# Optimization experiments

Measured on AMD Instinct MI355X. Metric: run time of the kernel, lower is better.

## Reference

```python
import jax, jax.numpy as jnp
import numpy as np

B, T, U = 64, 800, 80          # batch, stroke timesteps, char sequence length
IN, H, V = 3, 400, 57          # input_dim, hidden_dim, onehot_dim (vocab)
K, G = 10, 20                  # n_window, n_gaussian
D1 = H + IN + V                # input dim of recurrent layers >= 1


def setup_inputs() -> dict:
    key = jax.random.key(0)
    ks = jax.random.split(key, 12)
    std = 0.075
    nrm = lambda k, shp: (std * jax.random.normal(k, shp)).astype(jnp.float32)
    char_ids = jax.random.randint(ks[1], (B, U), 0, V)
    return {
        "x_input": jax.random.normal(ks[0], (B, T, IN), jnp.float32),
        "onehot": jax.nn.one_hot(char_ids, V, dtype=jnp.float32),
        "h0": jnp.zeros((B, H), jnp.float32),
        "h1": jnp.zeros((B, H), jnp.float32),
        "h2": jnp.zeros((B, H), jnp.float32),
        # GRU layer 0 (input: strokes only)
        "W_ih0": nrm(ks[2], (3 * H, IN)), "W_hh0": nrm(ks[3], (3 * H, H)),
        "b_ih0": jnp.zeros((3 * H,), jnp.float32), "b_hh0": jnp.zeros((3 * H,), jnp.float32),
        # GRU layer 1 (shared by all layers >= 1, faithful to the torch code which
        # always calls self.rnn_layer1 in the loop)
        "W_ih1": nrm(ks[4], (3 * H, D1)), "W_hh1": nrm(ks[5], (3 * H, H)),
        "b_ih1": jnp.zeros((3 * H,), jnp.float32), "b_hh1": jnp.zeros((3 * H,), jnp.float32),
        # attention window linear: hidden -> 3*K (alpha, beta, kappa); bias ~ N(-4, 0.1)
        "W_win": nrm(ks[6], (3 * K, H)),
        "b_win": (-4.0 + 0.1 * jax.random.normal(ks[7], (3 * K,))).astype(jnp.float32),
        # MDN head: hidden -> 1 + 6*G
        "W_mdn": nrm(ks[8], (1 + 6 * G, H)),
        "b_mdn": jnp.zeros((1 + 6 * G,), jnp.float32),
    }


def gru(x, h0, W_ih, W_hh, b_ih, b_hh):
    """PyTorch-convention GRU. x: (B,T,D), h0: (B,H) -> (out (B,T,H), hT (B,H))."""
    xg = jnp.einsum('btd,gd->btg', x, W_ih) + b_ih  # (B,T,3H), precomputed input gates

    def step(h, xg_t):
        gh = h @ W_hh.T + b_hh
        xr, xz, xn = jnp.split(xg_t, 3, axis=-1)
        hr, hz, hn = jnp.split(gh, 3, axis=-1)
        r = jax.nn.sigmoid(xr + hr)
        z = jax.nn.sigmoid(xz + hz)
        n = jnp.tanh(xn + r * hn)
        h_new = (1.0 - z) * n + z * h
        return h_new, h_new

    hT, outs = jax.lax.scan(step, h0, jnp.swapaxes(xg, 0, 1))
    return jnp.swapaxes(outs, 0, 1), hT


def reference(x_input, onehot, h0, h1, h2,
              W_ih0, W_hh0, b_ih0, b_hh0,
              W_ih1, W_hh1, b_ih1, b_hh1,
              W_win, b_win, W_mdn, b_mdn):
    out0, _ = gru(x_input, h0, W_ih0, W_hh0, b_ih0, b_hh0)  # (B,T,H)

    # Graves attention window (training=True path: running_kappa = cumsum(kappa))
    abk = jnp.exp(out0 @ W_win.T + b_win)                    # (B,T,3K)
    alpha, beta, kappa = jnp.split(abk, 3, axis=-1)          # each (B,T,K)
    running_kappa = jnp.cumsum(kappa, axis=1)                # (B,T,K)
    u = jnp.arange(onehot.shape[1], dtype=x_input.dtype)     # (U,)
    diff = running_kappa[..., None] - u                      # (B,T,K,U)
    phi = jnp.sum(alpha[..., None] * jnp.exp(-beta[..., None] * diff * diff), axis=2)  # (B,T,U)
    window = jnp.einsum('btu,buv->btv', phi, onehot)         # (B,T,V)

    # layers >= 1 all use layer-1 weights (faithful to original torch code)
    out = jnp.concatenate([out0, window, x_input], axis=-1)
    out, _ = gru(out, h1, W_ih1, W_hh1, b_ih1, b_hh1)
    out = jnp.concatenate([out, window, x_input], axis=-1)
    out, _ = gru(out, h2, W_ih1, W_hh1, b_ih1, b_hh1)

    mdn = out.reshape(-1, H) @ W_mdn.T + b_mdn               # (B*T, 1+6G)
    pi_logit = mdn[:, 0 * G:1 * G]
    mu1 = mdn[:, 1 * G:2 * G]
    mu2 = mdn[:, 2 * G:3 * G]
    log_sigma1 = mdn[:, 3 * G:4 * G]
    log_sigma2 = mdn[:, 4 * G:5 * G]
    rho = jnp.tanh(mdn[:, 5 * G:6 * G])
    e_logit = mdn[:, 6 * G:]
    return jnp.concatenate([pi_logit, mu1, mu2, log_sigma1, log_sigma2, rho, e_logit], axis=-1)
```

## Files before the change

### kernel.cpp

```cpp
#include <hip/hip_runtime.h>
#include <math.h>

#define Bx 64
#define Tx 800
#define Ux 80
#define INx 3
#define Hx 400
#define Vx 57
#define Kx 10


typedef float v2f __attribute__((ext_vector_type(2)));
typedef float v4f __attribute__((ext_vector_type(4)));

__device__ __forceinline__ float sigf(float x) { return 1.f / (1.f + expf(-x)); }

__device__ __forceinline__ void pk_lo(v2f& acc, v2f w, v2f h) {
    asm("v_pk_fma_f32 %0, %1, %2, %0 op_sel:[0,0,0] op_sel_hi:[0,1,1]"
        : "+v"(acc) : "v"(w), "v"(h));
}
__device__ __forceinline__ void pk_hi(v2f& acc, v2f w, v2f h) {
    asm("v_pk_fma_f32 %0, %1, %2, %0 op_sel:[1,0,0] op_sel_hi:[1,1,1]"
        : "+v"(acc) : "v"(w), "v"(h));
}

__global__ void k_zero(int* __restrict__ cnt) {
    int i = blockIdx.x * blockDim.x + threadIdx.x;
    if (i < 3 * 16 * 32) cnt[i] = 0;
}

__global__ void k_transpose_x(const float* __restrict__ x, float* __restrict__ xT) {
    int idx = blockIdx.x * blockDim.x + threadIdx.x;
    if (idx >= Tx * INx * Bx) return;
    int b = idx & 63;
    int d = (idx >> 6) % INx;
    int t = idx / (64 * INx);
    xT[idx] = x[((size_t)b * Tx + t) * INx + d];
}

__global__ void k_transpose_oh(const float* __restrict__ oh, float* __restrict__ ohT) {
    int idx = blockIdx.x * blockDim.x + threadIdx.x;
    if (idx >= Ux * Vx * Bx) return;
    int b = idx & 63;
    int uv = idx >> 6;
    int v = uv % Vx;
    int u = uv / Vx;
    ohT[idx] = oh[((size_t)b * Ux + u) * Vx + v];
}

__global__ void k_packW(const float* __restrict__ Whh, const float* __restrict__ Wih,
                        float* __restrict__ Wp, int NP, int xcols) {
    int idx = blockIdx.x * blockDim.x + threadIdx.x;
    int total = 16 * 3 * NP * 400;
    if (idx >= total) return;
    int q = idx % 400;
    int m = (idx / 400) % (3 * NP);
    int us = idx / (400 * 3 * NP);
    int g = m / NP, p = m % NP;
    int s = q / 25, u = q % 25;
    int row = g * 400 + us * 25 + u;
    float v0, v1;
    if (p < 13) {
        int kl0 = 2 * p, kl1 = 2 * p + 1;
        v0 = (kl0 < 25) ? Whh[(size_t)row * 400 + s * 25 + kl0] : 0.f;
        v1 = (kl1 < 25) ? Whh[(size_t)row * 400 + s * 25 + kl1] : 0.f;
    } else {
        int jx0 = 2 * (p - 13), jx1 = jx0 + 1;
        int kx0 = s * 29 + jx0, kx1 = s * 29 + jx1;
        v0 = (jx0 < 29 && kx0 < xcols) ? Wih[(size_t)row * xcols + kx0] : 0.f;
        v1 = (jx1 < 29 && kx1 < xcols) ? Wih[(size_t)row * xcols + kx1] : 0.f;
    }
    Wp[(size_t)idx * 2]     = v0;
    Wp[(size_t)idx * 2 + 1] = v1;
}

template <int XP>
__global__ __launch_bounds__(448, 2) void k_rec(
    const float* __restrict__ Wp, const float* __restrict__ prev,
    const float* __restrict__ winb, const float* __restrict__ xT,
    const float* __restrict__ hinit, const float* __restrict__ Wih_small,
    const float* __restrict__ bih, const float* __restrict__ bhh,
    float* __restrict__ outL, int* __restrict__ cnt) {
    constexpr int NP = 13 + XP;
    constexpr int XW = (XP > 0) ? 466 : 4;
    __shared__ __align__(16) float xcat_h[404 * 4];
    __shared__ __align__(16) float xcat_x[2][XW * 4];
    __shared__ v2f red2[8 * 400];
    __shared__ float biasLDS[150];
    __shared__ float wih0LDS[225];

    const int tid = threadIdx.x;
    const int us = blockIdx.x >> 4;
    const int cg = blockIdx.x & 15;
    const int cb = cg * 4;
    const int U0 = us * 25;
    const int q = tid;
    const int s = q / 25;
    int* cnt_cg = cnt + cg * 32;

    v2f w[3 * NP];
    if (q < 400) {
        const v2f* Wp2 = (const v2f*)Wp;
        #pragma unroll
        for (int m = 0; m < 3 * NP; ++m)
            w[m] = Wp2[((size_t)(us * 3 * NP) + m) * 400 + q];
    } else {
        #pragma unroll
        for (int m = 0; m < 3 * NP; ++m) w[m] = (v2f){0.f, 0.f};
    }
    if (tid < 75)        biasLDS[tid] = bih[(tid / 25) * 400 + U0 + (tid % 25)];
    else if (tid < 150)  biasLDS[tid] = bhh[((tid - 75) / 25) * 400 + U0 + ((tid - 75) % 25)];
    if (XP == 0 && tid < 225) {
        int u = tid / 9, r9 = tid % 9, g = r9 / 3, d = r9 % 3;
        wih0LDS[tid] = Wih_small[(size_t)(g * 400 + U0 + u) * 3 + d];
    }
    for (int k = tid; k < 404; k += 448)
        *(v4f*)&xcat_h[k * 4] = (v4f){0.f, 0.f, 0.f, 0.f};
    for (int k = tid; k < 2 * XW; k += 448)
        *(v4f*)&xcat_x[0][k * 4] = (v4f){0.f, 0.f, 0.f, 0.f};
    __syncthreads();

    if (XP > 0) {
        for (int kx = tid; kx < 460; kx += 448) {
            v4f xv;
            if (kx < 400)      xv = *(const v4f*)(prev + (size_t)kx * 64 + cb);
            else if (kx < 457) xv = *(const v4f*)(winb + (size_t)(kx - 400) * 64 + cb);
            else               xv = *(const v4f*)(xT + (size_t)(kx - 457) * 64 + cb);
            *(v4f*)&xcat_x[0][kx * 4] = xv;
        }
    } else {
        if (tid < 3)
            *(v4f*)&xcat_x[0][tid * 4] = *(const v4f*)(xT + (size_t)tid * 64 + cb);
    }

    for (int t = 0; t < Tx; ++t) {
        const int pl = t & 1;
        if (tid < 400) {
            v4f hv;
            if (t == 0) {
                hv.x = hinit[(size_t)(cb + 0) * 400 + tid];
                hv.y = hinit[(size_t)(cb + 1) * 400 + tid];
                hv.z = hinit[(size_t)(cb + 2) * 400 + tid];
                hv.w = hinit[(size_t)(cb + 3) * 400 + tid];
            } else {
                float* hp0 = outL + (size_t)(t - 1) * 25600 + (size_t)tid * 64 + cb;
                hv.x = __hip_atomic_load(hp0 + 0, __ATOMIC_RELAXED, __HIP_MEMORY_SCOPE_AGENT);
                hv.y = __hip_atomic_load(hp0 + 1, __ATOMIC_RELAXED, __HIP_MEMORY_SCOPE_AGENT);
                hv.z = __hip_atomic_load(hp0 + 2, __ATOMIC_RELAXED, __HIP_MEMORY_SCOPE_AGENT);
                hv.w = __hip_atomic_load(hp0 + 3, __ATOMIC_RELAXED, __HIP_MEMORY_SCOPE_AGENT);
            }
            *(v4f*)&xcat_h[tid * 4] = hv;
        }
        __syncthreads();

        if (q < 400) {
            v2f aR0 = {0, 0}, aR1 = {0, 0}, aZ0 = {0, 0}, aZ1 = {0, 0};
            v2f aHN0 = {0, 0}, aHN1 = {0, 0}, aXN0 = {0, 0}, aXN1 = {0, 0};
            const float* hb = &xcat_h[s * 100];
            #pragma unroll
            for (int p = 0; p < 13; ++p) {
                v2f a01 = *(const v2f*)(hb + 8 * p);
                v2f a23 = *(const v2f*)(hb + 8 * p + 2);
                v2f b01 = *(const v2f*)(hb + 8 * p + 4);
                v2f b23 = *(const v2f*)(hb + 8 * p + 6);
                v2f wr = w[p], wz = w[NP + p], wn = w[2 * NP + p];
                pk_lo(aR0, wr, a01);  pk_lo(aR1, wr, a23);
                pk_hi(aR0, wr, b01);  pk_hi(aR1, wr, b23);
                pk_lo(aZ0, wz, a01);  pk_lo(aZ1, wz, a23);
                pk_hi(aZ0, wz, b01);  pk_hi(aZ1, wz, b23);
                pk_lo(aHN0, wn, a01); pk_lo(aHN1, wn, a23);
                pk_hi(aHN0, wn, b01); pk_hi(aHN1, wn, b23);
            }
            if (XP > 0) {
                const float* xb = &xcat_x[pl][s * 29 * 4];
                #pragma unroll
                for (int p = 0; p < XP; ++p) {
                    v2f a01 = *(const v2f*)(xb + 8 * p);
                    v2f a23 = *(const v2f*)(xb + 8 * p + 2);
                    v2f b01 = *(const v2f*)(xb + 8 * p + 4);
                    v2f b23 = *(const v2f*)(xb + 8 * p + 6);
                    v2f wr = w[13 + p], wz = w[NP + 13 + p], wn = w[2 * NP + 13 + p];
                    pk_lo(aR0, wr, a01);  pk_lo(aR1, wr, a23);
                    pk_hi(aR0, wr, b01);  pk_hi(aR1, wr, b23);
                    pk_lo(aZ0, wz, a01);  pk_lo(aZ1, wz, a23);
                    pk_hi(aZ0, wz, b01);  pk_hi(aZ1, wz, b23);
                    pk_lo(aXN0, wn, a01); pk_lo(aXN1, wn, a23);
                    pk_hi(aXN0, wn, b01); pk_hi(aXN1, wn, b23);
                }
            }
            red2[0 * 400 + q] = aR0;  red2[1 * 400 + q] = aR1;
            red2[2 * 400 + q] = aZ0;  red2[3 * 400 + q] = aZ1;
            red2[4 * 400 + q] = aHN0; red2[5 * 400 + q] = aHN1;
            red2[6 * 400 + q] = aXN0; red2[7 * 400 + q] = aXN1;
        }
        __syncthreads();

        if (tid < 100) {
            int u = tid >> 2, c = tid & 3;
            int half = c >> 1, e = c & 1;
            const float* redf = (const float*)red2;
            float R = 0, Z = 0, HN = 0, XN = 0;
            #pragma unroll 4
            for (int s2 = 0; s2 < 16; ++s2) {
                int idx = s2 * 25 + u;
                R  += redf[((0 + half) * 400 + idx) * 2 + e];
                Z  += redf[((2 + half) * 400 + idx) * 2 + e];
                HN += redf[((4 + half) * 400 + idx) * 2 + e];
                XN += redf[((6 + half) * 400 + idx) * 2 + e];
            }
            R += biasLDS[u] + biasLDS[75 + u];
            Z += biasLDS[25 + u] + biasLDS[100 + u];
            XN += biasLDS[50 + u];
            HN += biasLDS[125 + u];
            if (XP == 0) {
                #pragma unroll
                for (int d = 0; d < 3; ++d) {
                    float xv = xcat_x[pl][d * 4 + c];
                    R  += wih0LDS[u * 9 + 0 + d] * xv;
                    Z  += wih0LDS[u * 9 + 3 + d] * xv;
                    XN += wih0LDS[u * 9 + 6 + d] * xv;
                }
            }
            float r = sigf(R);
            float z = sigf(Z);
            float n = tanhf(XN + r * HN);
            float hp = xcat_h[(U0 + u) * 4 + c];
            float hnew = (1.f - z) * n + z * hp;
            __hip_atomic_store(outL + (size_t)t * 25600 + (size_t)(U0 + u) * 64 + cb + c,
                               hnew, __ATOMIC_RELAXED, __HIP_MEMORY_SCOPE_AGENT);
        }

        if (t + 1 < Tx) {
            const int p2 = (t + 1) & 1;
            if (XP > 0) {
                for (int kx = tid; kx < 460; kx += 448) {
                    v4f xv;
                    if (kx < 400)      xv = *(const v4f*)(prev + (size_t)(t + 1) * 25600 + kx * 64 + cb);
                    else if (kx < 457) xv = *(const v4f*)(winb + (size_t)(t + 1) * 3648 + (kx - 400) * 64 + cb);
                    else               xv = *(const v4f*)(xT + (size_t)(t + 1) * 192 + (kx - 457) * 64 + cb);
                    *(v4f*)&xcat_x[p2][kx * 4] = xv;
                }
            } else {
                if (tid < 3)
                    *(v4f*)&xcat_x[p2][tid * 4] = *(const v4f*)(xT + (size_t)(t + 1) * 192 + tid * 64 + cb);
            }
        }
        __syncthreads();

        if (tid == 0) {
            __hip_atomic_fetch_add(cnt_cg, 1, __ATOMIC_RELAXED, __HIP_MEMORY_SCOPE_AGENT);
            int target = 16 * (t + 1);
            while (__hip_atomic_load(cnt_cg, __ATOMIC_RELAXED, __HIP_MEMORY_SCOPE_AGENT) < target)
                __builtin_amdgcn_s_sleep(2);
        }
        __syncthreads();
    }
}

__global__ __launch_bounds__(256) void k_abk(const float* __restrict__ out0,
    const float* __restrict__ Wwin, const float* __restrict__ bwin,
    float* __restrict__ abk) {
    int t = blockIdx.x;
    int b = threadIdx.x & 63;
    int js = threadIdx.x >> 6;
    int j0 = js * 8;
    int nj = min(8, 30 - j0);
    float acc[8];
    for (int i = 0; i < nj; i++) acc[i] = bwin[j0 + i];
    const float* o = out0 + (size_t)t * 25600;
    for (int k = 0; k < Hx; k++) {
        float hv = o[k * 64 + b];
        for (int i = 0; i < nj; i++) acc[i] += Wwin[(j0 + i) * Hx + k] * hv;
    }
    for (int i = 0; i < nj; i++)
        abk[(size_t)t * 1920 + (j0 + i) * 64 + b] = expf(acc[i]);
}

__global__ void k_cumsum(float* __restrict__ abk) {
    int tid = blockIdx.x * blockDim.x + threadIdx.x;
    if (tid >= Kx * Bx) return;
    int b = tid & 63;
    int k = tid >> 6;
    float run = 0.f;
    size_t base = (size_t)(20 + k) * 64 + b;
    for (int t = 0; t < Tx; t++) {
        size_t i = (size_t)t * 1920 + base;
        run += abk[i];
        abk[i] = run;
    }
}

__global__ __launch_bounds__(256) void k_window(const float* __restrict__ abk,
    const float* __restrict__ ohT, float* __restrict__ win) {
    int t = blockIdx.x;
    int b = threadIdx.x & 63;
    int sub = threadIdx.x >> 6;
    __shared__ float phi[Ux][64];

    float al[Kx], be[Kx], kc[Kx];
    const float* ab = abk + (size_t)t * 1920;
    #pragma unroll
    for (int k = 0; k < Kx; k++) {
        al[k] = ab[k * 64 + b];
        be[k] = ab[(10 + k) * 64 + b];
        kc[k] = ab[(20 + k) * 64 + b];
    }
    for (int u = sub * 20; u < sub * 20 + 20; u++) {
        float ssum = 0.f;
        float uf = (float)u;
        #pragma unroll
        for (int k = 0; k < Kx; k++) {
            float d = kc[k] - uf;
            ssum += al[k] * __expf(-be[k] * d * d);
        }
        phi[u][b] = ssum;
    }
    __syncthreads();

    int v0 = sub * 15;
    int nv = min(15, Vx - v0);
    float acc[15];
    for (int i = 0; i < nv; i++) acc[i] = 0.f;
    for (int u = 0; u < Ux; u++) {
        float pv = phi[u][b];
        const float* oh = ohT + (size_t)(u * Vx) * 64;
        for (int i = 0; i < nv; i++) acc[i] += pv * oh[(v0 + i) * 64 + b];
    }
    for (int i = 0; i < nv; i++)
        win[(size_t)t * 3648 + (v0 + i) * 64 + b] = acc[i];
}

__global__ __launch_bounds__(256) void k_mdn(const float* __restrict__ out2,
    const float* __restrict__ Wm, const float* __restrict__ bm,
    float* __restrict__ out) {
    int t = blockIdx.x;
    int b = threadIdx.x & 63;
    int js = threadIdx.x >> 6;
    int j0 = js * 31;
    int nj = min(31, 121 - j0);
    float acc[31];
    for (int i = 0; i < nj; i++) acc[i] = bm[j0 + i];
    const float* o = out2 + (size_t)t * 25600;
    for (int k = 0; k < Hx; k += 4) {
        float i0 = o[k * 64 + b];
        float i1 = o[(k + 1) * 64 + b];
        float i2 = o[(k + 2) * 64 + b];
        float i3 = o[(k + 3) * 64 + b];
        for (int i = 0; i < nj; i++) {
            const float* wp = Wm + (size_t)(j0 + i) * Hx + k;
            float4 qv = *(const float4*)wp;
            acc[i] += qv.x * i0 + qv.y * i1 + qv.z * i2 + qv.w * i3;
        }
    }
    size_t rb = ((size_t)b * Tx + t) * 121;
    for (int i = 0; i < nj; i++) {
        int j = j0 + i;
        float v = acc[i];
        if (j >= 100 && j < 120) v = tanhf(v);
        out[rb + j] = v;
    }
}

extern "C" void kernel_launch(void* const* d_in, const int* in_sizes, int n_in,
                              void* d_out, int out_size, void* d_ws, size_t ws_size,
                              hipStream_t stream) {
    const float* x    = (const float*)d_in[0];
    const float* oneh = (const float*)d_in[1];
    const float* h0i  = (const float*)d_in[2];
    const float* h1i  = (const float*)d_in[3];
    const float* h2i  = (const float*)d_in[4];
    const float* Wih0 = (const float*)d_in[5];
    const float* Whh0 = (const float*)d_in[6];
    const float* bih0 = (const float*)d_in[7];
    const float* bhh0 = (const float*)d_in[8];
    const float* Wih1 = (const float*)d_in[9];
    const float* Whh1 = (const float*)d_in[10];
    const float* bih1 = (const float*)d_in[11];
    const float* bhh1 = (const float*)d_in[12];
    const float* Wwin = (const float*)d_in[13];
    const float* bwin = (const float*)d_in[14];
    const float* Wmdn = (const float*)d_in[15];
    const float* bmdn = (const float*)d_in[16];

    float* ws    = (float*)d_ws;
    float* out0  = ws;
    float* out12 = ws + 20480000;
    float* winb  = ws + 40960000;
    float* abk   = ws + 43878400;
    float* xT    = ws + 45414400;
    float* ohT   = ws + 45568000;
    float* Wp0   = ws + 45859840;
    float* Wp12  = ws + 46359040;
    int*   cnt   = (int*)(ws + 47434240);

    hipLaunchKernelGGL(k_zero, dim3(6), dim3(256), 0, stream, cnt);
    hipLaunchKernelGGL(k_transpose_x, dim3((Tx * INx * Bx + 255) / 256), dim3(256), 0, stream, x, xT);
    hipLaunchKernelGGL(k_transpose_oh, dim3((Ux * Vx * Bx + 255) / 256), dim3(256), 0, stream, oneh, ohT);
    hipLaunchKernelGGL(k_packW, dim3((16 * 3 * 13 * 400 + 255) / 256), dim3(256), 0, stream,
                       Whh0, Wih0, Wp0, 13, 3);
    hipLaunchKernelGGL(k_packW, dim3((16 * 3 * 28 * 400 + 255) / 256), dim3(256), 0, stream,
                       Whh1, Wih1, Wp12, 28, 460);

    hipLaunchKernelGGL((k_rec<0>), dim3(256), dim3(448), 0, stream,
                       Wp0, (const float*)nullptr, (const float*)nullptr, xT,
                       h0i, Wih0, bih0, bhh0, out0, cnt + 0 * 512);

    hipLaunchKernelGGL(k_abk, dim3(Tx), dim3(256), 0, stream, out0, Wwin, bwin, abk);
    hipLaunchKernelGGL(k_cumsum, dim3(10), dim3(64), 0, stream, abk);
    hipLaunchKernelGGL(k_window, dim3(Tx), dim3(256), 0, stream, abk, ohT, winb);

    hipLaunchKernelGGL((k_rec<15>), dim3(256), dim3(448), 0, stream,
                       Wp12, out0, winb, xT, h1i, (const float*)nullptr,
                       bih1, bhh1, out12, cnt + 1 * 512);
    hipLaunchKernelGGL((k_rec<15>), dim3(256), dim3(448), 0, stream,
                       Wp12, out12, winb, xT, h2i, (const float*)nullptr,
                       bih1, bhh1, out0, cnt + 2 * 512);

    hipLaunchKernelGGL(k_mdn, dim3(Tx), dim3(256), 0, stream, out0, Wmdn, bmdn, (float*)d_out);
}
```

Baseline: 14.58 ms.

## Replace counter barrier with per-wave flag polling in recurrent GRU kernel

Replaces the per-step atomic-add counter and tid0 spin plus two block barriers with per-wave flags. The two compute waves each store the step index once their h outputs drain, and every wave polls all 32 flags with a wave vote before loading h. The previous h for the gate update now comes from a double-buffered LDS copy, and h is loaded with a cache-bypassing dwordx4. The next-step x prefetch moves to the otherwise idle waves so it overlaps the gate math. Launch bounds drop to one block per CU. This removes two __syncthreads per step and a contended atomic, at the cost of more subtle memory-ordering correctness.

After: 16.38 ms. +12.3%, slower.

```diff
diff --git a/kernel.cpp b/kernel.cpp
--- a/kernel.cpp
+++ b/kernel.cpp
@@ -75,7 +75,7 @@
 }
 
 template <int XP>
-__global__ __launch_bounds__(448, 2) void k_rec(
+__global__ __launch_bounds__(448, 1) void k_rec(
     const float* __restrict__ Wp, const float* __restrict__ prev,
     const float* __restrict__ winb, const float* __restrict__ xT,
     const float* __restrict__ hinit, const float* __restrict__ Wih_small,
@@ -85,6 +85,7 @@
     constexpr int XW = (XP > 0) ? 466 : 4;
     __shared__ __align__(16) float xcat_h[404 * 4];
     __shared__ __align__(16) float xcat_x[2][XW * 4];
+    __shared__ __align__(16) float hprev[2][104 * 4];
     __shared__ v2f red2[8 * 400];
     __shared__ float biasLDS[150];
     __shared__ float wih0LDS[225];
@@ -118,7 +119,6 @@
         *(v4f*)&xcat_h[k * 4] = (v4f){0.f, 0.f, 0.f, 0.f};
     for (int k = tid; k < 2 * XW; k += 448)
         *(v4f*)&xcat_x[0][k * 4] = (v4f){0.f, 0.f, 0.f, 0.f};
-    __syncthreads();
 
     if (XP > 0) {
         for (int kx = tid; kx < 460; kx += 448) {
@@ -135,6 +135,14 @@
 
     for (int t = 0; t < Tx; ++t) {
         const int pl = t & 1;
+        if (t > 0) {
+            int* fp = cnt_cg + (tid & 31);
+            int fv = __hip_atomic_load(fp, __ATOMIC_RELAXED, __HIP_MEMORY_SCOPE_AGENT);
+            while (!__all(fv >= t)) {
+                __builtin_amdgcn_s_sleep(1);
+                fv = __hip_atomic_load(fp, __ATOMIC_RELAXED, __HIP_MEMORY_SCOPE_AGENT);
+            }
+        }
         if (tid < 400) {
             v4f hv;
             if (t == 0) {
@@ -143,13 +151,14 @@
                 hv.z = hinit[(size_t)(cb + 2) * 400 + tid];
                 hv.w = hinit[(size_t)(cb + 3) * 400 + tid];
             } else {
-                float* hp0 = outL + (size_t)(t - 1) * 25600 + (size_t)tid * 64 + cb;
-                hv.x = __hip_atomic_load(hp0 + 0, __ATOMIC_RELAXED, __HIP_MEMORY_SCOPE_AGENT);
-                hv.y = __hip_atomic_load(hp0 + 1, __ATOMIC_RELAXED, __HIP_MEMORY_SCOPE_AGENT);
-                hv.z = __hip_atomic_load(hp0 + 2, __ATOMIC_RELAXED, __HIP_MEMORY_SCOPE_AGENT);
-                hv.w = __hip_atomic_load(hp0 + 3, __ATOMIC_RELAXED, __HIP_MEMORY_SCOPE_AGENT);
+                const float* hp0 = outL + (size_t)(t - 1) * 25600 + (size_t)tid * 64 + cb;
+                asm volatile("global_load_dwordx4 %0, %1, off sc0 sc1"
+                             : "=v"(hv) : "v"(hp0) : "memory");
+                asm volatile("s_waitcnt vmcnt(0)" ::: "memory");
             }
             *(v4f*)&xcat_h[tid * 4] = hv;
+            int d = tid - U0;
+            if ((unsigned)d < 25u) *(v4f*)&hprev[t & 1][d * 4] = hv;
         }
         __syncthreads();
 
@@ -195,45 +204,49 @@
         }
         __syncthreads();
 
-        if (tid < 100) {
-            int u = tid >> 2, c = tid & 3;
-            int half = c >> 1, e = c & 1;
-            const float* redf = (const float*)red2;
-            float R = 0, Z = 0, HN = 0, XN = 0;
-            #pragma unroll 4
-            for (int s2 = 0; s2 < 16; ++s2) {
-                int idx = s2 * 25 + u;
-                R  += redf[((0 + half) * 400 + idx) * 2 + e];
-                Z  += redf[((2 + half) * 400 + idx) * 2 + e];
-                HN += redf[((4 + half) * 400 + idx) * 2 + e];
-                XN += redf[((6 + half) * 400 + idx) * 2 + e];
-            }
-            R += biasLDS[u] + biasLDS[75 + u];
-            Z += biasLDS[25 + u] + biasLDS[100 + u];
-            XN += biasLDS[50 + u];
-            HN += biasLDS[125 + u];
-            if (XP == 0) {
-                #pragma unroll
-                for (int d = 0; d < 3; ++d) {
-                    float xv = xcat_x[pl][d * 4 + c];
-                    R  += wih0LDS[u * 9 + 0 + d] * xv;
-                    Z  += wih0LDS[u * 9 + 3 + d] * xv;
-                    XN += wih0LDS[u * 9 + 6 + d] * xv;
+        if (tid < 128) {
+            if (tid < 100) {
+                int u = tid >> 2, c = tid & 3;
+                int half = c >> 1, e = c & 1;
+                const float* redf = (const float*)red2;
+                float R = 0, Z = 0, HN = 0, XN = 0;
+                #pragma unroll 4
+                for (int s2 = 0; s2 < 16; ++s2) {
+                    int idx = s2 * 25 + u;
+                    R  += redf[((0 + half) * 400 + idx) * 2 + e];
+                    Z  += redf[((2 + half) * 400 + idx) * 2 + e];
+                    HN += redf[((4 + half) * 400 + idx) * 2 + e];
+                    XN += redf[((6 + half) * 400 + idx) * 2 + e];
                 }
-            }
-            float r = sigf(R);
-            float z = sigf(Z);
-            float n = tanhf(XN + r * HN);
-            float hp = xcat_h[(U0 + u) * 4 + c];
-            float hnew = (1.f - z) * n + z * hp;
-            __hip_atomic_store(outL + (size_t)t * 25600 + (size_t)(U0 + u) * 64 + cb + c,
-                               hnew, __ATOMIC_RELAXED, __HIP_MEMORY_SCOPE_AGENT);
-        }
-
-        if (t + 1 < Tx) {
+                R += biasLDS[u] + biasLDS[75 + u];
+                Z += biasLDS[25 + u] + biasLDS[100 + u];
+                XN += biasLDS[50 + u];
+                HN += biasLDS[125 + u];
+                if (XP == 0) {
+                    #pragma unroll
+                    for (int d = 0; d < 3; ++d) {
+                        float xv = xcat_x[pl][d * 4 + c];
+                        R  += wih0LDS[u * 9 + 0 + d] * xv;
+                        Z  += wih0LDS[u * 9 + 3 + d] * xv;
+                        XN += wih0LDS[u * 9 + 6 + d] * xv;
+                    }
+                }
+                float r = sigf(R);
+                float z = sigf(Z);
+                float n = tanhf(XN + r * HN);
+                float hp = hprev[t & 1][u * 4 + c];
+                float hnew = (1.f - z) * n + z * hp;
+                __hip_atomic_store(outL + (size_t)t * 25600 + (size_t)(U0 + u) * 64 + cb + c,
+                                   hnew, __ATOMIC_RELAXED, __HIP_MEMORY_SCOPE_AGENT);
+            }
+            asm volatile("s_waitcnt vmcnt(0)" ::: "memory");
+            if ((tid & 63) == 0)
+                __hip_atomic_store(cnt_cg + us * 2 + (tid >> 6), t + 1,
+                                   __ATOMIC_RELAXED, __HIP_MEMORY_SCOPE_AGENT);
+        } else if (t + 1 < Tx) {
             const int p2 = (t + 1) & 1;
             if (XP > 0) {
-                for (int kx = tid; kx < 460; kx += 448) {
+                for (int kx = tid - 128; kx < 460; kx += 320) {
                     v4f xv;
                     if (kx < 400)      xv = *(const v4f*)(prev + (size_t)(t + 1) * 25600 + kx * 64 + cb);
                     else if (kx < 457) xv = *(const v4f*)(winb + (size_t)(t + 1) * 3648 + (kx - 400) * 64 + cb);
@@ -241,19 +254,12 @@
                     *(v4f*)&xcat_x[p2][kx * 4] = xv;
                 }
             } else {
-                if (tid < 3)
-                    *(v4f*)&xcat_x[p2][tid * 4] = *(const v4f*)(xT + (size_t)(t + 1) * 192 + tid * 64 + cb);
-            }
-        }
-        __syncthreads();
-
-        if (tid == 0) {
-            __hip_atomic_fetch_add(cnt_cg, 1, __ATOMIC_RELAXED, __HIP_MEMORY_SCOPE_AGENT);
-            int target = 16 * (t + 1);
-            while (__hip_atomic_load(cnt_cg, __ATOMIC_RELAXED, __HIP_MEMORY_SCOPE_AGENT) < target)
-                __builtin_amdgcn_s_sleep(2);
-        }
-        __syncthreads();
+                if (tid < 131) {
+                    int d = tid - 128;
+                    *(v4f*)&xcat_x[p2][d * 4] = *(const v4f*)(xT + (size_t)(t + 1) * 192 + d * 64 + cb);
+                }
+            }
+        }
     }
 }
 
```
